# Kernel optimization log

Hardware: AMD Instinct MI355X
Metric: run time of the kernel (lower is better)

Reference implementation:

```python
import jax, jax.numpy as jnp
import numpy as np

E_REF = 2.0e11
I_REF = 1.0e-6
Q_REF = 1.0e3
L = 1.0
N = 262144
H = 64


def setup_inputs() -> dict:
    key = jax.random.key(0)
    ks = jax.random.split(key, 8)
    x = jax.random.uniform(ks[0], (N, 1), dtype=jnp.float32) * L
    E = (0.5 + jax.random.uniform(ks[1], (N, 1), dtype=jnp.float32)) * E_REF
    I = (0.5 + jax.random.uniform(ks[2], (N, 1), dtype=jnp.float32)) * I_REF
    q = (0.5 + jax.random.uniform(ks[3], (N, 1), dtype=jnp.float32)) * Q_REF

    def xavier(k, fin, fout):
        std = np.sqrt(2.0 / (fin + fout)).astype(np.float32)
        return jax.random.normal(k, (fin, fout), dtype=jnp.float32) * std

    return dict(
        x=x, E=E, I=I, q=q,
        W1=xavier(ks[4], 4, H), b1=jnp.zeros((H,), jnp.float32),
        W2=xavier(ks[5], H, H), b2=jnp.zeros((H,), jnp.float32),
        W3=xavier(ks[6], H, H), b3=jnp.zeros((H,), jnp.float32),
        W4=xavier(ks[7], H, 1), b4=jnp.zeros((1,), jnp.float32),
    )


def reference(x, E, I, q, W1, b1, W2, b2, W3, b3, W4, b4):
    # per-point scalar network psi(x; E, I, q)
    def psi_scalar(xs, feats):  # xs: scalar, feats: [3] = (E/E_ref, I/I_ref, q/q_ref)
        inp = jnp.concatenate([xs[None], feats])  # [4]
        h = jnp.tanh(inp @ W1 + b1)
        h = jnp.tanh(h @ W2 + b2)
        h = jnp.tanh(h @ W3 + b3)
        return (h @ W4 + b4)[0]

    d1 = jax.grad(psi_scalar)
    d2 = jax.grad(d1)
    d3 = jax.grad(d2)
    d4 = jax.grad(d3)

    feats = jnp.concatenate([E / E_REF, I / I_REF, q / Q_REF], axis=1)  # [N,3]
    xs = x[:, 0]  # [N]

    psi   = jax.vmap(psi_scalar)(xs, feats)[:, None]
    px    = jax.vmap(d1)(xs, feats)[:, None]
    pxx   = jax.vmap(d2)(xs, feats)[:, None]
    pxxx  = jax.vmap(d3)(xs, feats)[:, None]
    pxxxx = jax.vmap(d4)(xs, feats)[:, None]

    x2 = x * x
    w      = x2 * psi
    w_x    = 2 * x * psi + x2 * px
    w_xx   = 2 * psi + 4 * x * px + x2 * pxx
    w_xxx  = 6 * px + 6 * x * pxx + x2 * pxxx
    w_xxxx = 12 * pxx + 8 * x * pxxx + x2 * pxxxx

    eps = jnp.finfo(x.dtype).eps
    s = q * L ** 4 / (E * I + eps)
    # stacked outputs: [5, N, 1] = (w, w_x, w_xx, w_xxx, w_xxxx)
    return jnp.stack([
        s * w,
        s * (w_x / L),
        s * (w_xx / L ** 2),
        s * (w_xxx / L ** 3),
        s * (w_xxxx / L ** 4),
    ])
```

## Files before the change

kernel.cpp:

```cpp
#include <hip/hip_runtime.h>
#include <stdint.h>

typedef _Float16 f16x2 __attribute__((ext_vector_type(2)));
typedef _Float16 f16x4 __attribute__((ext_vector_type(4)));
typedef _Float16 f16x8 __attribute__((ext_vector_type(8)));
typedef __fp16   hf16x2 __attribute__((ext_vector_type(2)));
typedef float    f32x4 __attribute__((ext_vector_type(4)));
typedef uint4    u128a __attribute__((may_alias));

union HU   { uint32_t u; _Float16 h[2]; };
union B128 { uint4 q; f16x8 v; };
union PK2  { hf16x2 a; f16x2 b; };

__device__ __forceinline__ f16x2 pkrtz2(float lo, float hi) {
  PK2 u; u.a = __builtin_amdgcn_cvt_pkrtz(lo, hi);
  return u.b;
}

__device__ __forceinline__ f16x8 cat4(f16x2 a, f16x2 b, f16x2 c, f16x2 d) {
  f16x4 ab = __builtin_shufflevector(a, b, 0, 1, 2, 3);
  f16x4 cd = __builtin_shufflevector(c, d, 0, 1, 2, 3);
  return __builtin_shufflevector(ab, cd, 0, 1, 2, 3, 4, 5, 6, 7);
}

__device__ __forceinline__ float fast_exp2(float x) {
#if __has_builtin(__builtin_amdgcn_exp2f)
  return __builtin_amdgcn_exp2f(x);
#else
  return exp2f(x);
#endif
}
__device__ __forceinline__ float fast_rcp(float x) {
#if __has_builtin(__builtin_amdgcn_rcpf)
  return __builtin_amdgcn_rcpf(x);
#else
  return 1.0f / x;
#endif
}

__device__ __forceinline__ void tanh_jets(float u0, float u1, float u2, float u3, float u4,
                                          float& t0, float& t1, float& t2, float& t3, float& t4) {
  float aa = fminf(fmaf(2.8853900817779268f, u0, 2.0f), 127.0f);
  float e4 = fast_exp2(aa);
  float r  = fast_rcp(fmaf(0.25f, e4, 1.0f));
  t0 = fmaf(-2.0f, r, 1.0f);
  float v0 = e4 * (r * r);
  t1 = v0 * u1;
  float h1 = t0 * t1;
  t2 = fmaf(u2, v0, -(u1 * h1));
  float v2 = -fmaf(t0 + t0, t2, t1 * t1);
  t3 = fmaf(u3, v0, fmaf(-1.3333333333f * u2, h1, 0.3333333333f * u1 * v2));
  float v3 = -2.0f * fmaf(t0, t3, t1 * t2);
  t4 = fmaf(u4, v0, fmaf(-1.5f * u3, h1, fmaf(0.5f * u2, v2, 0.25f * u1 * v3)));
}

__device__ __forceinline__ void tanh_jets1(float u0, float u1,
                                           float& t0, float& t1, float& t2, float& t3, float& t4) {
  float aa = fminf(fmaf(2.8853900817779268f, u0, 2.0f), 127.0f);
  float e4 = fast_exp2(aa);
  float r  = fast_rcp(fmaf(0.25f, e4, 1.0f));
  t0 = fmaf(-2.0f, r, 1.0f);
  float v0 = e4 * (r * r);
  t1 = v0 * u1;
  float h1 = t0 * t1;
  t2 = -(u1 * h1);
  float v2 = -fmaf(t0 + t0, t2, t1 * t1);
  t3 = 0.3333333333f * (u1 * v2);
  float v3 = -2.0f * fmaf(t0, t3, t1 * t2);
  t4 = 0.25f * (u1 * v3);
}

__global__ void prep_kernel(const float* __restrict__ W1, const float* __restrict__ b1,
                            const float* __restrict__ W2, const float* __restrict__ W3,
                            const float* __restrict__ W4, uint32_t* __restrict__ ws) {
  const int t = threadIdx.x;
  float* P1 = (float*)ws;
  if (t < 64) {
    P1[t * 8 + 0] = W1[0 * 64 + t];
    P1[t * 8 + 1] = W1[1 * 64 + t];
    P1[t * 8 + 2] = W1[2 * 64 + t];
    P1[t * 8 + 3] = W1[3 * 64 + t];
    P1[t * 8 + 4] = b1[t];
    P1[t * 8 + 5] = 0.f; P1[t * 8 + 6] = 0.f; P1[t * 8 + 7] = 0.f;
  }
  for (int idx = t; idx < 2048; idx += 256) {
    const int fi = idx >> 8;
    const int tm = fi >> 1, s = fi & 1;
    const int l  = (idx >> 2) & 63;
    const int pj = idx & 3;
    const int g  = l >> 4;
    const int mm = 16 * tm + (l & 15);
    const int j0 = 2 * pj, j1 = 2 * pj + 1;
    const int k2a = 16 * g + 8 * s + j0;
    const int k2b = 16 * g + 8 * s + j1;
    HU a; a.h[0] = (_Float16)W2[k2a * 64 + mm]; a.h[1] = (_Float16)W2[k2b * 64 + mm];
    ws[512 + idx] = a.u;
    const int k3a = 32 * s + 16 * (j0 >> 2) + 4 * g + (j0 & 3);
    const int k3b = 32 * s + 16 * (j1 >> 2) + 4 * g + (j1 & 3);
    HU b; b.h[0] = (_Float16)W3[k3a * 64 + mm]; b.h[1] = (_Float16)W3[k3b * 64 + mm];
    ws[2560 + idx] = b.u;
  }
  if (t < 64) {
    ws[4608 + t] = __float_as_uint(W4[t]);
  }
}

#define MFMA16(A, B, C) __builtin_amdgcn_mfma_f32_16x16x32_f16((A), (B), (C), 0, 0, 0)

#define MM5(AF, TM, S, BF) { \
    acc[0][TM] = MFMA16((AF).v, BF[0][S], acc[0][TM]); \
    acc[1][TM] = MFMA16((AF).v, BF[1][S], acc[1][TM]); \
    acc[2][TM] = MFMA16((AF).v, BF[2][S], acc[2][TM]); \
    acc[3][TM] = MFMA16((AF).v, BF[3][S], acc[3][TM]); \
    acc[4][TM] = MFMA16((AF).v, BF[4][S], acc[4][TM]); }

#define L1P(S, DI, D0, D1, D2, D3, D4) { \
  const int h0_ = 16 * g + 8 * (S) + 2 * (DI); \
  float A0_, A1_, A2_, A3_, A4_, B0_, B1_, B2_, B3_, B4_; \
  { const float4 wv_ = *(const float4*)(P1f + h0_ * 8); \
    const float bb_  = P1f[h0_ * 8 + 4]; \
    float u0_ = fmaf(wv_.x, x, fmaf(wv_.y, f1, fmaf(wv_.z, f2, fmaf(wv_.w, f3, bb_)))); \
    tanh_jets1(u0_, wv_.x, A0_, A1_, A2_, A3_, A4_); } \
  { const float4 wv_ = *(const float4*)(P1f + (h0_ + 1) * 8); \
    const float bb_  = P1f[(h0_ + 1) * 8 + 4]; \
    float u0_ = fmaf(wv_.x, x, fmaf(wv_.y, f1, fmaf(wv_.z, f2, fmaf(wv_.w, f3, bb_)))); \
    tanh_jets1(u0_, wv_.x, B0_, B1_, B2_, B3_, B4_); } \
  D0 = pkrtz2(A0_, B0_); D1 = pkrtz2(A1_, B1_); D2 = pkrtz2(A2_, B2_); \
  D3 = pkrtz2(A3_, B3_); D4 = pkrtz2(A4_, B4_); }

#define L1HALF(S) { \
  f16x2 qa0, qa1, qa2, qa3, qa4, qb0, qb1, qb2, qb3, qb4; \
  f16x2 qc0, qc1, qc2, qc3, qc4, qd0, qd1, qd2, qd3, qd4; \
  L1P(S, 0, qa0, qa1, qa2, qa3, qa4) \
  L1P(S, 1, qb0, qb1, qb2, qb3, qb4) \
  L1P(S, 2, qc0, qc1, qc2, qc3, qc4) \
  L1P(S, 3, qd0, qd1, qd2, qd3, qd4) \
  bf2[0][S] = cat4(qa0, qb0, qc0, qd0); \
  bf2[1][S] = cat4(qa1, qb1, qc1, qd1); \
  bf2[2][S] = cat4(qa2, qb2, qc2, qd2); \
  bf2[3][S] = cat4(qa3, qb3, qc3, qd3); \
  bf2[4][S] = cat4(qa4, qb4, qc4, qd4); }

#define PKTILE(TM, E0, E1, E2, E3, E4, F0, F1, F2, F3, F4) { \
  float A0_, A1_, A2_, A3_, A4_, B0_, B1_, B2_, B3_, B4_; \
  tanh_jets(acc[0][TM][0], acc[1][TM][0], acc[2][TM][0], acc[3][TM][0], acc[4][TM][0], \
            A0_, A1_, A2_, A3_, A4_); \
  tanh_jets(acc[0][TM][1], acc[1][TM][1], acc[2][TM][1], acc[3][TM][1], acc[4][TM][1], \
            B0_, B1_, B2_, B3_, B4_); \
  E0 = pkrtz2(A0_, B0_); E1 = pkrtz2(A1_, B1_); E2 = pkrtz2(A2_, B2_); \
  E3 = pkrtz2(A3_, B3_); E4 = pkrtz2(A4_, B4_); \
  tanh_jets(acc[0][TM][2], acc[1][TM][2], acc[2][TM][2], acc[3][TM][2], acc[4][TM][2], \
            A0_, A1_, A2_, A3_, A4_); \
  tanh_jets(acc[0][TM][3], acc[1][TM][3], acc[2][TM][3], acc[3][TM][3], acc[4][TM][3], \
            B0_, B1_, B2_, B3_, B4_); \
  F0 = pkrtz2(A0_, B0_); F1 = pkrtz2(A1_, B1_); F2 = pkrtz2(A2_, B2_); \
  F3 = pkrtz2(A3_, B3_); F4 = pkrtz2(A4_, B4_); }

#define PKHALF(S2) { \
  f16x2 ve0, ve1, ve2, ve3, ve4, vf0, vf1, vf2, vf3, vf4; \
  f16x2 vm0, vm1, vm2, vm3, vm4, vn0, vn1, vn2, vn3, vn4; \
  PKTILE(2 * (S2),     ve0, ve1, ve2, ve3, ve4, vf0, vf1, vf2, vf3, vf4) \
  PKTILE(2 * (S2) + 1, vm0, vm1, vm2, vm3, vm4, vn0, vn1, vn2, vn3, vn4) \
  bf3[0][S2] = cat4(ve0, vf0, vm0, vn0); \
  bf3[1][S2] = cat4(ve1, vf1, vm1, vn1); \
  bf3[2][S2] = cat4(ve2, vf2, vm2, vn2); \
  bf3[3][S2] = cat4(ve3, vf3, vm3, vn3); \
  bf3[4][S2] = cat4(ve4, vf4, vm4, vn4); }

__global__ __launch_bounds__(64, 3)
void beam_kernel(const float* __restrict__ X, const float* __restrict__ Ein,
                 const float* __restrict__ Iin, const float* __restrict__ Qin,
                 const float* __restrict__ b2, const float* __restrict__ b3,
                 const float* __restrict__ b4, const uint32_t* __restrict__ ws,
                 float* __restrict__ out, int n) {
  const int l   = threadIdx.x & 63;
  const int g   = l >> 4;
  const int p   = l & 15;
  int i = blockIdx.x * 16 + p;
  if (i >= n) i = n - 1;

  const float x  = X[i];
  const float Ev = Ein[i], Iv = Iin[i], qv = Qin[i];
  const float f1 = Ev * 5.0e-12f;
  const float f2 = Iv * 1.0e6f;
  const float f3 = qv * 1.0e-3f;
  const float sf = qv * fast_rcp(fmaf(Ev, Iv, 1.1920929e-7f));

  const float* P1f = (const float*)ws;
  const float* W4f = (const float*)(ws + 4608);

  B128 A20, A21, A22, A23, A24, A25, A26, A27;
  A20.q = *(const u128a*)(ws + 512 + ((0) * 64 + l) * 4);
  A21.q = *(const u128a*)(ws + 512 + ((1) * 64 + l) * 4);
  A22.q = *(const u128a*)(ws + 512 + ((2) * 64 + l) * 4);
  A23.q = *(const u128a*)(ws + 512 + ((3) * 64 + l) * 4);
  A24.q = *(const u128a*)(ws + 512 + ((4) * 64 + l) * 4);
  A25.q = *(const u128a*)(ws + 512 + ((5) * 64 + l) * 4);
  A26.q = *(const u128a*)(ws + 512 + ((6) * 64 + l) * 4);
  A27.q = *(const u128a*)(ws + 512 + ((7) * 64 + l) * 4);

  f16x8 bf2[5][2];
  L1HALF(0)
  L1HALF(1)

  f32x4 acc[5][4];
  #pragma unroll
  for (int tm = 0; tm < 4; ++tm) {
    const float4 bv = *(const float4*)(b2 + 16 * tm + 4 * g);
    acc[0][tm] = (f32x4){bv.x, bv.y, bv.z, bv.w};
    #pragma unroll
    for (int k = 1; k < 5; ++k) acc[k][tm] = (f32x4){0.f, 0.f, 0.f, 0.f};
  }
  MM5(A20, 0, 0, bf2) MM5(A22, 1, 0, bf2) MM5(A24, 2, 0, bf2) MM5(A26, 3, 0, bf2)
  MM5(A21, 0, 1, bf2) MM5(A23, 1, 1, bf2) MM5(A25, 2, 1, bf2) MM5(A27, 3, 1, bf2)

  B128 A30, A31, A32, A33, A34, A35, A36, A37;
  A30.q = *(const u128a*)(ws + 2560 + ((0) * 64 + l) * 4);
  A31.q = *(const u128a*)(ws + 2560 + ((1) * 64 + l) * 4);
  A32.q = *(const u128a*)(ws + 2560 + ((2) * 64 + l) * 4);
  A33.q = *(const u128a*)(ws + 2560 + ((3) * 64 + l) * 4);
  A34.q = *(const u128a*)(ws + 2560 + ((4) * 64 + l) * 4);
  A35.q = *(const u128a*)(ws + 2560 + ((5) * 64 + l) * 4);
  A36.q = *(const u128a*)(ws + 2560 + ((6) * 64 + l) * 4);
  A37.q = *(const u128a*)(ws + 2560 + ((7) * 64 + l) * 4);

  f16x8 bf3[5][2];
  PKHALF(0)
  PKHALF(1)

  #pragma unroll
  for (int tm = 0; tm < 4; ++tm) {
    const float4 bv = *(const float4*)(b3 + 16 * tm + 4 * g);
    acc[0][tm] = (f32x4){bv.x, bv.y, bv.z, bv.w};
    #pragma unroll
    for (int k = 1; k < 5; ++k) acc[k][tm] = (f32x4){0.f, 0.f, 0.f, 0.f};
  }
  MM5(A30, 0, 0, bf3) MM5(A32, 1, 0, bf3) MM5(A34, 2, 0, bf3) MM5(A36, 3, 0, bf3)
  MM5(A31, 0, 1, bf3) MM5(A33, 1, 1, bf3) MM5(A35, 2, 1, bf3) MM5(A37, 3, 1, bf3)

  float w4f[16];
  #pragma unroll
  for (int tm = 0; tm < 4; ++tm) {
    const float4 wv = *(const float4*)(W4f + 16 * tm + 4 * g);
    w4f[4 * tm + 0] = wv.x; w4f[4 * tm + 1] = wv.y;
    w4f[4 * tm + 2] = wv.z; w4f[4 * tm + 3] = wv.w;
  }

  #pragma unroll
  for (int tm = 0; tm < 4; ++tm) {
    #pragma unroll
    for (int r = 0; r < 4; ++r) {
      float t0, t1, t2, t3, t4;
      tanh_jets(acc[0][tm][r], acc[1][tm][r], acc[2][tm][r], acc[3][tm][r], acc[4][tm][r],
                t0, t1, t2, t3, t4);
      acc[0][tm][r] = t0; acc[1][tm][r] = t1; acc[2][tm][r] = t2;
      acc[3][tm][r] = t3; acc[4][tm][r] = t4;
    }
  }

  float zz[5] = {0.f, 0.f, 0.f, 0.f, 0.f};
  #pragma unroll
  for (int tm = 0; tm < 4; ++tm) {
    #pragma unroll
    for (int k = 0; k < 5; ++k) {
      zz[k] = fmaf(w4f[4 * tm + 0], acc[k][tm][0], zz[k]);
      zz[k] = fmaf(w4f[4 * tm + 1], acc[k][tm][1], zz[k]);
      zz[k] = fmaf(w4f[4 * tm + 2], acc[k][tm][2], zz[k]);
      zz[k] = fmaf(w4f[4 * tm + 3], acc[k][tm][3], zz[k]);
    }
  }
  #pragma unroll
  for (int k = 0; k < 5; ++k) {
    zz[k] += __shfl_xor(zz[k], 16, 64);
    zz[k] += __shfl_xor(zz[k], 32, 64);
  }

  const float psi   = zz[0] + b4[0];
  const float px    = zz[1];
  const float pxx   = 2.0f  * zz[2];
  const float pxxx  = 6.0f  * zz[3];
  const float pxxxx = 24.0f * zz[4];
  const float x2 = x * x;
  const float o0 = sf * (x2 * psi);
  const float o1 = sf * fmaf(2.0f * x, psi, x2 * px);
  const float o2 = sf * (fmaf(4.0f * x, px, 2.0f * psi) + x2 * pxx);
  const float o3 = sf * (fmaf(6.0f * x, pxx, 6.0f * px) + x2 * pxxx);
  const float o4 = sf * (fmaf(8.0f * x, pxxx, 12.0f * pxx) + x2 * pxxxx);
  const float og = (g == 0) ? o0 : (g == 1) ? o1 : (g == 2) ? o2 : o3;
  out[g * n + i] = og;
  if (l < 16) out[4 * n + i] = o4;
}

extern "C" void kernel_launch(void* const* d_in, const int* in_sizes, int n_in,
                              void* d_out, int out_size, void* d_ws, size_t ws_size,
                              hipStream_t stream) {
  const float* X  = (const float*)d_in[0];
  const float* E  = (const float*)d_in[1];
  const float* I  = (const float*)d_in[2];
  const float* q  = (const float*)d_in[3];
  const float* W1 = (const float*)d_in[4];
  const float* b1 = (const float*)d_in[5];
  const float* W2 = (const float*)d_in[6];
  const float* b2 = (const float*)d_in[7];
  const float* W3 = (const float*)d_in[8];
  const float* b3 = (const float*)d_in[9];
  const float* W4 = (const float*)d_in[10];
  const float* b4 = (const float*)d_in[11];
  const int n = in_sizes[0];
  uint32_t* ws = (uint32_t*)d_ws;
  float* out = (float*)d_out;

  prep_kernel<<<dim3(1), dim3(256), 0, stream>>>(W1, b1, W2, W3, W4, ws);
  beam_kernel<<<dim3((n + 15) / 16), dim3(64), 0, stream>>>(X, E, I, q, b2, b3, b4, ws, out, n);
}
```

Measured before the change: 60.00 us.

## Split MFMA layers into half-tiles to shrink accumulators and raise occupancy

Layers 2 and 3 are now processed in two halves of output rows. Each half loads only four A fragments, runs its MFMAs into a 5x2 accumulator and immediately applies the tanh-jet epilogue before the next half. The final layer's W4 dot product is fused into the layer-3 epilogue. This cuts live VGPRs (accumulators plus A fragments), and launch_bounds goes from 3 to 4 waves per EU. The cost is less MFMA/VALU overlap within a wave and more serialization between MFMA and tanh phases.

```diff
diff --git a/kernel.cpp b/kernel.cpp
--- a/kernel.cpp
+++ b/kernel.cpp
@@ -107,12 +107,22 @@
 
 #define MFMA16(A, B, C) __builtin_amdgcn_mfma_f32_16x16x32_f16((A), (B), (C), 0, 0, 0)
 
-#define MM5(AF, TM, S, BF) { \
-    acc[0][TM] = MFMA16((AF).v, BF[0][S], acc[0][TM]); \
-    acc[1][TM] = MFMA16((AF).v, BF[1][S], acc[1][TM]); \
-    acc[2][TM] = MFMA16((AF).v, BF[2][S], acc[2][TM]); \
-    acc[3][TM] = MFMA16((AF).v, BF[3][S], acc[3][TM]); \
-    acc[4][TM] = MFMA16((AF).v, BF[4][S], acc[4][TM]); }
+#define MM5H(AF, T, S, BF) { \
+    acc[0][T] = MFMA16((AF).v, BF[0][S], acc[0][T]); \
+    acc[1][T] = MFMA16((AF).v, BF[1][S], acc[1][T]); \
+    acc[2][T] = MFMA16((AF).v, BF[2][S], acc[2][T]); \
+    acc[3][T] = MFMA16((AF).v, BF[3][S], acc[3][T]); \
+    acc[4][T] = MFMA16((AF).v, BF[4][S], acc[4][T]); }
+
+#define INIT2(BIAS, HH) { \
+  const float4 bv0_ = *(const float4*)((BIAS) + 16 * (2 * (HH) + 0) + 4 * g); \
+  const float4 bv1_ = *(const float4*)((BIAS) + 16 * (2 * (HH) + 1) + 4 * g); \
+  acc[0][0] = (f32x4){bv0_.x, bv0_.y, bv0_.z, bv0_.w}; \
+  acc[0][1] = (f32x4){bv1_.x, bv1_.y, bv1_.z, bv1_.w}; \
+  acc[1][0] = (f32x4){0.f, 0.f, 0.f, 0.f}; acc[1][1] = (f32x4){0.f, 0.f, 0.f, 0.f}; \
+  acc[2][0] = (f32x4){0.f, 0.f, 0.f, 0.f}; acc[2][1] = (f32x4){0.f, 0.f, 0.f, 0.f}; \
+  acc[3][0] = (f32x4){0.f, 0.f, 0.f, 0.f}; acc[3][1] = (f32x4){0.f, 0.f, 0.f, 0.f}; \
+  acc[4][0] = (f32x4){0.f, 0.f, 0.f, 0.f}; acc[4][1] = (f32x4){0.f, 0.f, 0.f, 0.f}; }
 
 #define L1P(S, DI, D0, D1, D2, D3, D4) { \
   const int h0_ = 16 * g + 8 * (S) + 2 * (DI); \
@@ -141,33 +151,57 @@
   bf2[3][S] = cat4(qa3, qb3, qc3, qd3); \
   bf2[4][S] = cat4(qa4, qb4, qc4, qd4); }
 
-#define PKTILE(TM, E0, E1, E2, E3, E4, F0, F1, F2, F3, F4) { \
+#define PKTILE2(T, E0, E1, E2, E3, E4, F0, F1, F2, F3, F4) { \
   float A0_, A1_, A2_, A3_, A4_, B0_, B1_, B2_, B3_, B4_; \
-  tanh_jets(acc[0][TM][0], acc[1][TM][0], acc[2][TM][0], acc[3][TM][0], acc[4][TM][0], \
+  tanh_jets(acc[0][T][0], acc[1][T][0], acc[2][T][0], acc[3][T][0], acc[4][T][0], \
             A0_, A1_, A2_, A3_, A4_); \
-  tanh_jets(acc[0][TM][1], acc[1][TM][1], acc[2][TM][1], acc[3][TM][1], acc[4][TM][1], \
+  tanh_jets(acc[0][T][1], acc[1][T][1], acc[2][T][1], acc[3][T][1], acc[4][T][1], \
             B0_, B1_, B2_, B3_, B4_); \
   E0 = pkrtz2(A0_, B0_); E1 = pkrtz2(A1_, B1_); E2 = pkrtz2(A2_, B2_); \
   E3 = pkrtz2(A3_, B3_); E4 = pkrtz2(A4_, B4_); \
-  tanh_jets(acc[0][TM][2], acc[1][TM][2], acc[2][TM][2], acc[3][TM][2], acc[4][TM][2], \
+  tanh_jets(acc[0][T][2], acc[1][T][2], acc[2][T][2], acc[3][T][2], acc[4][T][2], \
             A0_, A1_, A2_, A3_, A4_); \
-  tanh_jets(acc[0][TM][3], acc[1][TM][3], acc[2][TM][3], acc[3][TM][3], acc[4][TM][3], \
+  tanh_jets(acc[0][T][3], acc[1][T][3], acc[2][T][3], acc[3][T][3], acc[4][T][3], \
             B0_, B1_, B2_, B3_, B4_); \
   F0 = pkrtz2(A0_, B0_); F1 = pkrtz2(A1_, B1_); F2 = pkrtz2(A2_, B2_); \
   F3 = pkrtz2(A3_, B3_); F4 = pkrtz2(A4_, B4_); }
 
-#define PKHALF(S2) { \
+#define PKHALF2(HH) { \
   f16x2 ve0, ve1, ve2, ve3, ve4, vf0, vf1, vf2, vf3, vf4; \
   f16x2 vm0, vm1, vm2, vm3, vm4, vn0, vn1, vn2, vn3, vn4; \
-  PKTILE(2 * (S2),     ve0, ve1, ve2, ve3, ve4, vf0, vf1, vf2, vf3, vf4) \
-  PKTILE(2 * (S2) + 1, vm0, vm1, vm2, vm3, vm4, vn0, vn1, vn2, vn3, vn4) \
-  bf3[0][S2] = cat4(ve0, vf0, vm0, vn0); \
-  bf3[1][S2] = cat4(ve1, vf1, vm1, vn1); \
-  bf3[2][S2] = cat4(ve2, vf2, vm2, vn2); \
-  bf3[3][S2] = cat4(ve3, vf3, vm3, vn3); \
-  bf3[4][S2] = cat4(ve4, vf4, vm4, vn4); }
-
-__global__ __launch_bounds__(64, 3)
+  PKTILE2(0, ve0, ve1, ve2, ve3, ve4, vf0, vf1, vf2, vf3, vf4) \
+  PKTILE2(1, vm0, vm1, vm2, vm3, vm4, vn0, vn1, vn2, vn3, vn4) \
+  bf3[0][HH] = cat4(ve0, vf0, vm0, vn0); \
+  bf3[1][HH] = cat4(ve1, vf1, vm1, vn1); \
+  bf3[2][HH] = cat4(ve2, vf2, vm2, vn2); \
+  bf3[3][HH] = cat4(ve3, vf3, vm3, vn3); \
+  bf3[4][HH] = cat4(ve4, vf4, vm4, vn4); }
+
+#define L3T(T, TMG) { \
+  const float4 wv4_ = *(const float4*)(W4f + 16 * (TMG) + 4 * g); \
+  float t0_, t1_, t2_, t3_, t4_; \
+  tanh_jets(acc[0][T][0], acc[1][T][0], acc[2][T][0], acc[3][T][0], acc[4][T][0], \
+            t0_, t1_, t2_, t3_, t4_); \
+  zz[0] = fmaf(wv4_.x, t0_, zz[0]); zz[1] = fmaf(wv4_.x, t1_, zz[1]); \
+  zz[2] = fmaf(wv4_.x, t2_, zz[2]); zz[3] = fmaf(wv4_.x, t3_, zz[3]); \
+  zz[4] = fmaf(wv4_.x, t4_, zz[4]); \
+  tanh_jets(acc[0][T][1], acc[1][T][1], acc[2][T][1], acc[3][T][1], acc[4][T][1], \
+            t0_, t1_, t2_, t3_, t4_); \
+  zz[0] = fmaf(wv4_.y, t0_, zz[0]); zz[1] = fmaf(wv4_.y, t1_, zz[1]); \
+  zz[2] = fmaf(wv4_.y, t2_, zz[2]); zz[3] = fmaf(wv4_.y, t3_, zz[3]); \
+  zz[4] = fmaf(wv4_.y, t4_, zz[4]); \
+  tanh_jets(acc[0][T][2], acc[1][T][2], acc[2][T][2], acc[3][T][2], acc[4][T][2], \
+            t0_, t1_, t2_, t3_, t4_); \
+  zz[0] = fmaf(wv4_.z, t0_, zz[0]); zz[1] = fmaf(wv4_.z, t1_, zz[1]); \
+  zz[2] = fmaf(wv4_.z, t2_, zz[2]); zz[3] = fmaf(wv4_.z, t3_, zz[3]); \
+  zz[4] = fmaf(wv4_.z, t4_, zz[4]); \
+  tanh_jets(acc[0][T][3], acc[1][T][3], acc[2][T][3], acc[3][T][3], acc[4][T][3], \
+            t0_, t1_, t2_, t3_, t4_); \
+  zz[0] = fmaf(wv4_.w, t0_, zz[0]); zz[1] = fmaf(wv4_.w, t1_, zz[1]); \
+  zz[2] = fmaf(wv4_.w, t2_, zz[2]); zz[3] = fmaf(wv4_.w, t3_, zz[3]); \
+  zz[4] = fmaf(wv4_.w, t4_, zz[4]); }
+
+__global__ __launch_bounds__(64, 4)
 void beam_kernel(const float* __restrict__ X, const float* __restrict__ Ein,
                  const float* __restrict__ Iin, const float* __restrict__ Qin,
                  const float* __restrict__ b2, const float* __restrict__ b3,
@@ -189,86 +223,61 @@
   const float* P1f = (const float*)ws;
   const float* W4f = (const float*)(ws + 4608);
 
-  B128 A20, A21, A22, A23, A24, A25, A26, A27;
-  A20.q = *(const u128a*)(ws + 512 + ((0) * 64 + l) * 4);
-  A21.q = *(const u128a*)(ws + 512 + ((1) * 64 + l) * 4);
-  A22.q = *(const u128a*)(ws + 512 + ((2) * 64 + l) * 4);
-  A23.q = *(const u128a*)(ws + 512 + ((3) * 64 + l) * 4);
-  A24.q = *(const u128a*)(ws + 512 + ((4) * 64 + l) * 4);
-  A25.q = *(const u128a*)(ws + 512 + ((5) * 64 + l) * 4);
-  A26.q = *(const u128a*)(ws + 512 + ((6) * 64 + l) * 4);
-  A27.q = *(const u128a*)(ws + 512 + ((7) * 64 + l) * 4);
-
   f16x8 bf2[5][2];
   L1HALF(0)
   L1HALF(1)
 
-  f32x4 acc[5][4];
-  #pragma unroll
-  for (int tm = 0; tm < 4; ++tm) {
-    const float4 bv = *(const float4*)(b2 + 16 * tm + 4 * g);
-    acc[0][tm] = (f32x4){bv.x, bv.y, bv.z, bv.w};
-    #pragma unroll
-    for (int k = 1; k < 5; ++k) acc[k][tm] = (f32x4){0.f, 0.f, 0.f, 0.f};
-  }
-  MM5(A20, 0, 0, bf2) MM5(A22, 1, 0, bf2) MM5(A24, 2, 0, bf2) MM5(A26, 3, 0, bf2)
-  MM5(A21, 0, 1, bf2) MM5(A23, 1, 1, bf2) MM5(A25, 2, 1, bf2) MM5(A27, 3, 1, bf2)
-
-  B128 A30, A31, A32, A33, A34, A35, A36, A37;
-  A30.q = *(const u128a*)(ws + 2560 + ((0) * 64 + l) * 4);
-  A31.q = *(const u128a*)(ws + 2560 + ((1) * 64 + l) * 4);
-  A32.q = *(const u128a*)(ws + 2560 + ((2) * 64 + l) * 4);
-  A33.q = *(const u128a*)(ws + 2560 + ((3) * 64 + l) * 4);
-  A34.q = *(const u128a*)(ws + 2560 + ((4) * 64 + l) * 4);
-  A35.q = *(const u128a*)(ws + 2560 + ((5) * 64 + l) * 4);
-  A36.q = *(const u128a*)(ws + 2560 + ((6) * 64 + l) * 4);
-  A37.q = *(const u128a*)(ws + 2560 + ((7) * 64 + l) * 4);
-
   f16x8 bf3[5][2];
-  PKHALF(0)
-  PKHALF(1)
-
-  #pragma unroll
-  for (int tm = 0; tm < 4; ++tm) {
-    const float4 bv = *(const float4*)(b3 + 16 * tm + 4 * g);
-    acc[0][tm] = (f32x4){bv.x, bv.y, bv.z, bv.w};
-    #pragma unroll
-    for (int k = 1; k < 5; ++k) acc[k][tm] = (f32x4){0.f, 0.f, 0.f, 0.f};
-  }
-  MM5(A30, 0, 0, bf3) MM5(A32, 1, 0, bf3) MM5(A34, 2, 0, bf3) MM5(A36, 3, 0, bf3)
-  MM5(A31, 0, 1, bf3) MM5(A33, 1, 1, bf3) MM5(A35, 2, 1, bf3) MM5(A37, 3, 1, bf3)
-
-  float w4f[16];
-  #pragma unroll
-  for (int tm = 0; tm < 4; ++tm) {
-    const float4 wv = *(const float4*)(W4f + 16 * tm + 4 * g);
-    w4f[4 * tm + 0] = wv.x; w4f[4 * tm + 1] = wv.y;
-    w4f[4 * tm + 2] = wv.z; w4f[4 * tm + 3] = wv.w;
-  }
-
-  #pragma unroll
-  for (int tm = 0; tm < 4; ++tm) {
-    #pragma unroll
-    for (int r = 0; r < 4; ++r) {
-      float t0, t1, t2, t3, t4;
-      tanh_jets(acc[0][tm][r], acc[1][tm][r], acc[2][tm][r], acc[3][tm][r], acc[4][tm][r],
-                t0, t1, t2, t3, t4);
-      acc[0][tm][r] = t0; acc[1][tm][r] = t1; acc[2][tm][r] = t2;
-      acc[3][tm][r] = t3; acc[4][tm][r] = t4;
-    }
+  f32x4 acc[5][2];
+  {
+    B128 Fa, Fb, Fc, Fd;
+    Fa.q = *(const u128a*)(ws + 512 + ((0) * 64 + l) * 4);
+    Fb.q = *(const u128a*)(ws + 512 + ((1) * 64 + l) * 4);
+    Fc.q = *(const u128a*)(ws + 512 + ((2) * 64 + l) * 4);
+    Fd.q = *(const u128a*)(ws + 512 + ((3) * 64 + l) * 4);
+    INIT2(b2, 0)
+    MM5H(Fa, 0, 0, bf2) MM5H(Fc, 1, 0, bf2)
+    MM5H(Fb, 0, 1, bf2) MM5H(Fd, 1, 1, bf2)
+    PKHALF2(0)
+  }
+  {
+    B128 Fa, Fb, Fc, Fd;
+    Fa.q = *(const u128a*)(ws + 512 + ((4) * 64 + l) * 4);
+    Fb.q = *(const u128a*)(ws + 512 + ((5) * 64 + l) * 4);
+    Fc.q = *(const u128a*)(ws + 512 + ((6) * 64 + l) * 4);
+    Fd.q = *(const u128a*)(ws + 512 + ((7) * 64 + l) * 4);
+    INIT2(b2, 1)
+    MM5H(Fa, 0, 0, bf2) MM5H(Fc, 1, 0, bf2)
+    MM5H(Fb, 0, 1, bf2) MM5H(Fd, 1, 1, bf2)
+    PKHALF2(1)
   }
 
   float zz[5] = {0.f, 0.f, 0.f, 0.f, 0.f};
-  #pragma unroll
-  for (int tm = 0; tm < 4; ++tm) {
-    #pragma unroll
-    for (int k = 0; k < 5; ++k) {
-      zz[k] = fmaf(w4f[4 * tm + 0], acc[k][tm][0], zz[k]);
-      zz[k] = fmaf(w4f[4 * tm + 1], acc[k][tm][1], zz[k]);
-      zz[k] = fmaf(w4f[4 * tm + 2], acc[k][tm][2], zz[k]);
-      zz[k] = fmaf(w4f[4 * tm + 3], acc[k][tm][3], zz[k]);
-    }
-  }
+  {
+    B128 Fa, Fb, Fc, Fd;
+    Fa.q = *(const u128a*)(ws + 2560 + ((0) * 64 + l) * 4);
+    Fb.q = *(const u128a*)(ws + 2560 + ((1) * 64 + l) * 4);
+    Fc.q = *(const u128a*)(ws + 2560 + ((2) * 64 + l) * 4);
+    Fd.q = *(const u128a*)(ws + 2560 + ((3) * 64 + l) * 4);
+    INIT2(b3, 0)
+    MM5H(Fa, 0, 0, bf3) MM5H(Fc, 1, 0, bf3)
+    MM5H(Fb, 0, 1, bf3) MM5H(Fd, 1, 1, bf3)
+    L3T(0, 0)
+    L3T(1, 1)
+  }
+  {
+    B128 Fa, Fb, Fc, Fd;
+    Fa.q = *(const u128a*)(ws + 2560 + ((4) * 64 + l) * 4);
+    Fb.q = *(const u128a*)(ws + 2560 + ((5) * 64 + l) * 4);
+    Fc.q = *(const u128a*)(ws + 2560 + ((6) * 64 + l) * 4);
+    Fd.q = *(const u128a*)(ws + 2560 + ((7) * 64 + l) * 4);
+    INIT2(b3, 1)
+    MM5H(Fa, 0, 0, bf3) MM5H(Fc, 1, 0, bf3)
+    MM5H(Fb, 0, 1, bf3) MM5H(Fd, 1, 1, bf3)
+    L3T(0, 2)
+    L3T(1, 3)
+  }
+
   #pragma unroll
   for (int k = 0; k < 5; ++k) {
     zz[k] += __shfl_xor(zz[k], 16, 64);
```

Measured after the change: 59.82 us. No clear change (-0.3%).
